# Optimization experiments

Measured on AMD Instinct MI355X. Metric: run time of the kernel, lower is better.

Reference implementation:

```python
import jax, jax.numpy as jnp
import numpy as np


def setup_inputs() -> dict:
    key = jax.random.key(0)
    k1, k2 = jax.random.split(key)
    B, T, V = 128, 256, 256
    batch = jax.random.normal(k1, (B, T, V, 3), dtype=jnp.float32)
    missing = jax.random.uniform(k2, (B, T, V)) < 0.2
    labels = jnp.where(missing, -1.0, 1.0)
    batch = batch.at[..., 0].set(labels)
    return {"batch": batch}


def reference(batch):
    B, T, V, _ = batch.shape
    dt = batch.dtype
    # constant-velocity model matrices (hardcoded in the module)
    F = jnp.array([[1, 0, 1, 0], [0, 1, 0, 1], [0, 0, 1, 0], [0, 0, 0, 1]], dtype=dt)
    H = jnp.array([[1, 0, 0, 0], [0, 1, 0, 0]], dtype=dt)
    Q = jnp.eye(4, dtype=dt) * 0.01
    R = jnp.eye(2, dtype=dt) * 1.0
    I4 = jnp.eye(4, dtype=dt)

    s0 = jnp.zeros((B, V, 4), dtype=dt)
    P0 = jnp.broadcast_to(jnp.eye(4, dtype=dt) * 1000.0, (B, V, 4, 4))

    obs_t = jnp.moveaxis(batch, 1, 0)  # (T, B, V, 3)

    def step(carry, obs):
        s, P = carry  # s: (B,V,4), P: (B,V,4,4)
        labels = obs[..., 0]
        z = obs[..., 1:]                       # (B,V,2)
        mask = (labels != -1)[..., None]       # (B,V,1)
        s_pred = jnp.einsum('bvj,ij->bvi', s, F)                 # s @ F.T
        P_pred = jnp.einsum('ij,bvjk,lk->bvil', F, P, F) + Q     # F P F^T + Q
        y = (z - s_pred[..., :2]) * mask                          # (B,V,2)
        S = P_pred[..., :2, :2] + R                               # H P H^T + R
        K = jnp.einsum('bvij,bvjk->bvik', P_pred[..., :, :2], jnp.linalg.inv(S))  # (B,V,4,2)
        s_upd = s_pred + jnp.einsum('bvij,bvj->bvi', K, y) * mask
        KH = jnp.einsum('bvij,jk->bvik', K, H)                    # (B,V,4,4)
        P_upd = jnp.einsum('bvij,bvjk->bvik', I4 - KH, P_pred)
        s_new = jnp.where(mask, s_upd, s_pred)
        P_new = jnp.where(mask[..., None], P_upd, P_pred)
        return (s_new, P_new), None

    (s_final, _), _ = jax.lax.scan(step, (s0, P0), obs_t)
    last_pos = s_final[..., :2]                                   # (B,V,2)
    ones = jnp.ones((B, V, 1), dtype=dt)
    return jnp.concatenate((ones, last_pos), axis=-1)             # (B,V,3)
```

## Files before the change

### kernel.cpp

```cpp
#include <hip/hip_runtime.h>
#include <stdint.h>


#define KF_B 128
#define KF_T 256
#define KF_V 256

typedef float f4 __attribute__((ext_vector_type(4)));

#define GLOAD(dst, sbase, imm)                                         \
    asm volatile("global_load_dwordx4 %0, %1, %2 offset:" #imm         \
                 : "=v"(dst) : "v"(voff), "s"(sbase) : "memory")

#define WAITVM(N, B)                                                   \
    asm volatile("s_waitcnt vmcnt(" #N ")"                             \
                 : "+v"((B)[0]), "+v"((B)[1]),                         \
                   "+v"((B)[2]), "+v"((B)[3]) :: "memory")

#define KF_ISSUE(buf)                          \
    do {                                       \
        GLOAD((buf)[0], sb0, 0);               \
        GLOAD((buf)[1], sb0, 3072);            \
        GLOAD((buf)[2], sb1, 0);               \
        GLOAD((buf)[3], sb1, 3068);            \
        sb0 += 12288; sb1 += 12288;            \
    } while (0)

#define KF_STEP3(label, z0, z1)                                         \
    do {                                                                \
                                                           \
        const float xp0 = x0 + v0;                                      \
        const float xp1 = x1 + v1;                                      \
        const float q00 = p00 + 2.f * p01 + p11 + 0.01f;                \
        const float q01 = p01 + p11;                                    \
        const float q11 = p11 + 0.01f;                                  \
                       \
        const float S = q00 + 1.f;                                      \
        const float m = ((label) != -1.0f) ? 1.0f : 0.0f;               \
        const float is = m * __builtin_amdgcn_rcpf(S);                  \
        const float K0 = q00 * is;                                      \
        const float K1 = q01 * is;                                      \
                                   \
        const float y0 = (z0) - xp0;                                    \
        const float y1 = (z1) - xp1;                                    \
        x0 = xp0 + K0 * y0;                                             \
        v0 = v0 + K1 * y0;                                              \
        x1 = xp1 + K0 * y1;                                             \
        v1 = v1 + K1 * y1;                                              \
                                                 \
        p00 = q00 - K0 * q00;                                           \
        p01 = q01 - K0 * q01;                                           \
        p11 = q11 - K1 * q01;                                           \
    } while (0)

#define KF_CONSUME(B)                                        \
    do {                                                     \
        KF_STEP3((B)[0][0], (B)[0][1], (B)[0][2]);           \
        KF_STEP3((B)[1][0], (B)[1][1], (B)[1][2]);           \
        KF_STEP3((B)[2][0], (B)[2][1], (B)[2][2]);           \
        KF_STEP3((B)[3][1], (B)[3][2], (B)[3][3]);           \
    } while (0)

__global__ __launch_bounds__(64, 1) void kf_kernel(const float* __restrict__ batch,
                                                   float* __restrict__ out) {
    const int blk = blockIdx.x;
    const int b = blk >> 2;
    const int v = ((blk & 3) << 6) | threadIdx.x;

    const uint32_t voff = (uint32_t)v * 12u;
    uint64_t sb0 = (uint64_t)batch + (uint64_t)b * (KF_T * KF_V * 3 * 4);
    uint64_t sb1 = sb0 + 6144;

    float p00 = 1000.f, p01 = 0.f, p11 = 1000.f;
    float x0 = 0.f, v0 = 0.f;
    float x1 = 0.f, v1 = 0.f;

#pragma unroll 1
    for (int body = 0; body < 16; ++body) {
        f4 g0[4], g1[4], g2[4], g3[4];
        KF_ISSUE(g0);
        KF_ISSUE(g1);
        KF_ISSUE(g2);
        KF_ISSUE(g3);
        WAITVM(12, g0); KF_CONSUME(g0);
        WAITVM(8,  g1); KF_CONSUME(g1);
        WAITVM(4,  g2); KF_CONSUME(g2);
        WAITVM(0,  g3); KF_CONSUME(g3);
    }

    const int tid = blk * 64 + threadIdx.x;
    float* o = out + (size_t)tid * 3;
    o[0] = 1.0f;
    o[1] = x0;
    o[2] = x1;
}

extern "C" void kernel_launch(void* const* d_in, const int* in_sizes, int n_in,
                              void* d_out, int out_size, void* d_ws, size_t ws_size,
                              hipStream_t stream) {
    (void)in_sizes; (void)n_in; (void)d_ws; (void)ws_size; (void)out_size;
    const float* batch = (const float*)d_in[0];
    float* out = (float*)d_out;
    const int total = KF_B * KF_V;
    kf_kernel<<<total / 64, 64, 0, stream>>>(batch, out);
}
```

Before: 146.1 us.

## Replace batched load/consume loop with rolling 8-deep software pipeline

Replaces the loop that issued four load groups and then drained all of them with a fully unrolled rolling pipeline of eight buffers. Each steady-state stage waits for its oldest group, consumes it, then immediately reissues loads into that buffer, so 32 loads stay in flight at all times instead of draining to zero every 16 timesteps. Total timesteps stay at 256 (8 prologue, 56 steady, 8 epilogue stages). The cost is higher VGPR use for 8 buffers and a much larger unrolled code body.

```diff
diff --git a/kernel.cpp b/kernel.cpp
--- a/kernel.cpp
+++ b/kernel.cpp
@@ -61,6 +61,14 @@
         KF_STEP3((B)[3][1], (B)[3][2], (B)[3][3]);           \
     } while (0)
 
+#define KF_STEADY(B)  do { WAITVM(28, B); KF_CONSUME(B); KF_ISSUE(B); } while (0)
+#define KF_STEADY8()                                          \
+    do {                                                      \
+        KF_STEADY(b0); KF_STEADY(b1); KF_STEADY(b2);          \
+        KF_STEADY(b3); KF_STEADY(b4); KF_STEADY(b5);          \
+        KF_STEADY(b6); KF_STEADY(b7);                         \
+    } while (0)
+
 __global__ __launch_bounds__(64, 1) void kf_kernel(const float* __restrict__ batch,
                                                    float* __restrict__ out) {
     const int blk = blockIdx.x;
@@ -75,18 +83,27 @@
     float x0 = 0.f, v0 = 0.f;
     float x1 = 0.f, v1 = 0.f;
 
-#pragma unroll 1
-    for (int body = 0; body < 16; ++body) {
-        f4 g0[4], g1[4], g2[4], g3[4];
-        KF_ISSUE(g0);
-        KF_ISSUE(g1);
-        KF_ISSUE(g2);
-        KF_ISSUE(g3);
-        WAITVM(12, g0); KF_CONSUME(g0);
-        WAITVM(8,  g1); KF_CONSUME(g1);
-        WAITVM(4,  g2); KF_CONSUME(g2);
-        WAITVM(0,  g3); KF_CONSUME(g3);
-    }
+    f4 b0[4], b1[4], b2[4], b3[4], b4[4], b5[4], b6[4], b7[4];
+
+    KF_ISSUE(b0); KF_ISSUE(b1); KF_ISSUE(b2); KF_ISSUE(b3);
+    KF_ISSUE(b4); KF_ISSUE(b5); KF_ISSUE(b6); KF_ISSUE(b7);
+
+    KF_STEADY8();
+    KF_STEADY8();
+    KF_STEADY8();
+    KF_STEADY8();
+    KF_STEADY8();
+    KF_STEADY8();
+    KF_STEADY8();
+
+    WAITVM(28, b0); KF_CONSUME(b0);
+    WAITVM(24, b1); KF_CONSUME(b1);
+    WAITVM(20, b2); KF_CONSUME(b2);
+    WAITVM(16, b3); KF_CONSUME(b3);
+    WAITVM(12, b4); KF_CONSUME(b4);
+    WAITVM(8,  b5); KF_CONSUME(b5);
+    WAITVM(4,  b6); KF_CONSUME(b6);
+    WAITVM(0,  b7); KF_CONSUME(b7);
 
     const int tid = blk * 64 + threadIdx.x;
     float* o = out + (size_t)tid * 3;
```

Result: no change. 144.5 us (-1.1%).

## Split Kalman time scan into four segments composed via affine maps

Applied to the files above, without the earlier changes.

Each block now uses four waves, each handling a quarter of the time axis for 64 spatial columns. The first wave runs the filter directly. The others first warm up the covariance recursion for 32 steps, then accumulate their segment's state update as an affine map, which is written to shared memory and composed by wave 0. This is meant to cut the long serial latency chain of the per-thread scan. It adds redundant covariance work and scalar loads in place of the old hand-scheduled vector loads. It also relies on the covariance converging within the warm-up window, so it is approximate if long runs of missing observations occur.

```diff
diff --git a/kernel.cpp b/kernel.cpp
--- a/kernel.cpp
+++ b/kernel.cpp
@@ -5,94 +5,139 @@
 #define KF_B 128
 #define KF_T 256
 #define KF_V 256
+#define SEGLEN 64
+#define WARM 32
+#define STRIDE (KF_V * 3)
 
-typedef float f4 __attribute__((ext_vector_type(4)));
+#define KF_GAIN(la)                                                  \
+    const float q00 = p00 + 2.f * p01 + p11 + 0.01f;                 \
+    const float q01 = p01 + p11;                                     \
+    const float q11 = p11 + 0.01f;                                   \
+    const float m = ((la) != -1.0f) ? 1.0f : 0.0f;                   \
+    const float is = m * __builtin_amdgcn_rcpf(q00 + 1.f);           \
+    const float K0 = q00 * is;                                       \
+    const float K1 = q01 * is;                                       \
+    p00 = q00 - K0 * q00;                                            \
+    p01 = q01 - K0 * q01;                                            \
+    p11 = q11 - K1 * q01;
 
-#define GLOAD(dst, sbase, imm)                                         \
-    asm volatile("global_load_dwordx4 %0, %1, %2 offset:" #imm         \
-                 : "=v"(dst) : "v"(voff), "s"(sbase) : "memory")
-
-#define WAITVM(N, B)                                                   \
-    asm volatile("s_waitcnt vmcnt(" #N ")"                             \
-                 : "+v"((B)[0]), "+v"((B)[1]),                         \
-                   "+v"((B)[2]), "+v"((B)[3]) :: "memory")
-
-#define KF_ISSUE(buf)                          \
-    do {                                       \
-        GLOAD((buf)[0], sb0, 0);               \
-        GLOAD((buf)[1], sb0, 3072);            \
-        GLOAD((buf)[2], sb1, 0);               \
-        GLOAD((buf)[3], sb1, 3068);            \
-        sb0 += 12288; sb1 += 12288;            \
+#define STEP_DIR(la, z0, z1)                                         \
+    do {                                                             \
+        KF_GAIN(la)                                                  \
+        const float xp0 = x0 + v0;                                   \
+        const float xp1 = x1 + v1;                                   \
+        const float y0 = (z0) - xp0;                                 \
+        const float y1 = (z1) - xp1;                                 \
+        x0 = xp0 + K0 * y0;                                          \
+        v0 = v0 + K1 * y0;                                           \
+        x1 = xp1 + K0 * y1;                                          \
+        v1 = v1 + K1 * y1;                                           \
     } while (0)
 
-#define KF_STEP3(label, z0, z1)                                         \
-    do {                                                                \
-                                                           \
-        const float xp0 = x0 + v0;                                      \
-        const float xp1 = x1 + v1;                                      \
-        const float q00 = p00 + 2.f * p01 + p11 + 0.01f;                \
-        const float q01 = p01 + p11;                                    \
-        const float q11 = p11 + 0.01f;                                  \
-                       \
-        const float S = q00 + 1.f;                                      \
-        const float m = ((label) != -1.0f) ? 1.0f : 0.0f;               \
-        const float is = m * __builtin_amdgcn_rcpf(S);                  \
-        const float K0 = q00 * is;                                      \
-        const float K1 = q01 * is;                                      \
-                                   \
-        const float y0 = (z0) - xp0;                                    \
-        const float y1 = (z1) - xp1;                                    \
-        x0 = xp0 + K0 * y0;                                             \
-        v0 = v0 + K1 * y0;                                              \
-        x1 = xp1 + K0 * y1;                                             \
-        v1 = v1 + K1 * y1;                                              \
-                                                 \
-        p00 = q00 - K0 * q00;                                           \
-        p01 = q01 - K0 * q01;                                           \
-        p11 = q11 - K1 * q01;                                           \
+#define STEP_AFF(la, z0, z1)                                         \
+    do {                                                             \
+        KF_GAIN(la)                                                  \
+        const float s00 = a00 + a10;                                 \
+        const float s01 = a01 + a11;                                 \
+        a00 = s00 - K0 * s00;                                        \
+        a01 = s01 - K0 * s01;                                        \
+        a10 = a10 - K1 * s00;                                        \
+        a11 = a11 - K1 * s01;                                        \
+        const float sbx = bx0 + bx1;                                 \
+        const float sby = by0 + by1;                                 \
+        bx0 = sbx + K0 * ((z0) - sbx);                               \
+        bx1 = bx1 + K1 * ((z0) - sbx);                               \
+        by0 = sby + K0 * ((z1) - sby);                               \
+        by1 = by1 + K1 * ((z1) - sby);                               \
     } while (0)
 
-#define KF_CONSUME(B)                                        \
-    do {                                                     \
-        KF_STEP3((B)[0][0], (B)[0][1], (B)[0][2]);           \
-        KF_STEP3((B)[1][0], (B)[1][1], (B)[1][2]);           \
-        KF_STEP3((B)[2][0], (B)[2][1], (B)[2][2]);           \
-        KF_STEP3((B)[3][1], (B)[3][2], (B)[3][3]);           \
-    } while (0)
+#define STEP_RICC(la)                                                \
+    do { KF_GAIN(la) } while (0)
 
-__global__ __launch_bounds__(64, 1) void kf_kernel(const float* __restrict__ batch,
-                                                   float* __restrict__ out) {
+__global__ __launch_bounds__(256, 4)
+void kf_kernel(const float* __restrict__ batch, float* __restrict__ out) {
     const int blk = blockIdx.x;
     const int b = blk >> 2;
-    const int v = ((blk & 3) << 6) | threadIdx.x;
+    const int lane = threadIdx.x & 63;
+    const int w = threadIdx.x >> 6;
+    const int v = ((blk & 3) << 6) | lane;
 
-    const uint32_t voff = (uint32_t)v * 12u;
-    uint64_t sb0 = (uint64_t)batch + (uint64_t)b * (KF_T * KF_V * 3 * 4);
-    uint64_t sb1 = sb0 + 6144;
+    const float* col = batch + (size_t)b * (KF_T * STRIDE) + (size_t)v * 3;
+
+    __shared__ float lds[3][64][9];
 
     float p00 = 1000.f, p01 = 0.f, p11 = 1000.f;
-    float x0 = 0.f, v0 = 0.f;
-    float x1 = 0.f, v1 = 0.f;
+    float x0 = 0.f, v0 = 0.f, x1 = 0.f, v1 = 0.f;
+    float a00 = 1.f, a01 = 0.f, a10 = 0.f, a11 = 1.f;
+    float bx0 = 0.f, bx1 = 0.f, by0 = 0.f, by1 = 0.f;
 
+    if (w == 0) {
+        const float* p = col;
+#pragma unroll 2
+        for (int t = 0; t < SEGLEN; t += 4) {
+            const float la0 = p[0],          z00 = p[1],          z01 = p[2];
+            const float la1 = p[STRIDE],     z10 = p[STRIDE+1],   z11 = p[STRIDE+2];
+            const float la2 = p[2*STRIDE],   z20 = p[2*STRIDE+1], z21 = p[2*STRIDE+2];
+            const float la3 = p[3*STRIDE],   z30 = p[3*STRIDE+1], z31 = p[3*STRIDE+2];
+            p += 4 * STRIDE;
+            STEP_DIR(la0, z00, z01);
+            STEP_DIR(la1, z10, z11);
+            STEP_DIR(la2, z20, z21);
+            STEP_DIR(la3, z30, z31);
+        }
+    } else {
+        const float* p = col + (size_t)(w * SEGLEN - WARM) * STRIDE;
 #pragma unroll 1
-    for (int body = 0; body < 16; ++body) {
-        f4 g0[4], g1[4], g2[4], g3[4];
-        KF_ISSUE(g0);
-        KF_ISSUE(g1);
-        KF_ISSUE(g2);
-        KF_ISSUE(g3);
-        WAITVM(12, g0); KF_CONSUME(g0);
-        WAITVM(8,  g1); KF_CONSUME(g1);
-        WAITVM(4,  g2); KF_CONSUME(g2);
-        WAITVM(0,  g3); KF_CONSUME(g3);
+        for (int t = 0; t < WARM; t += 8) {
+            const float la0 = p[0];
+            const float la1 = p[STRIDE];
+            const float la2 = p[2*STRIDE];
+            const float la3 = p[3*STRIDE];
+            const float la4 = p[4*STRIDE];
+            const float la5 = p[5*STRIDE];
+            const float la6 = p[6*STRIDE];
+            const float la7 = p[7*STRIDE];
+            p += 8 * STRIDE;
+            STEP_RICC(la0); STEP_RICC(la1); STEP_RICC(la2); STEP_RICC(la3);
+            STEP_RICC(la4); STEP_RICC(la5); STEP_RICC(la6); STEP_RICC(la7);
+        }
+#pragma unroll 2
+        for (int t = 0; t < SEGLEN; t += 4) {
+            const float la0 = p[0],          z00 = p[1],          z01 = p[2];
+            const float la1 = p[STRIDE],     z10 = p[STRIDE+1],   z11 = p[STRIDE+2];
+            const float la2 = p[2*STRIDE],   z20 = p[2*STRIDE+1], z21 = p[2*STRIDE+2];
+            const float la3 = p[3*STRIDE],   z30 = p[3*STRIDE+1], z31 = p[3*STRIDE+2];
+            p += 4 * STRIDE;
+            STEP_AFF(la0, z00, z01);
+            STEP_AFF(la1, z10, z11);
+            STEP_AFF(la2, z20, z21);
+            STEP_AFF(la3, z30, z31);
+        }
+        float* q = lds[w - 1][lane];
+        q[0] = a00; q[1] = a01; q[2] = a10; q[3] = a11;
+        q[4] = bx0; q[5] = bx1; q[6] = by0; q[7] = by1;
     }
 
-    const int tid = blk * 64 + threadIdx.x;
-    float* o = out + (size_t)tid * 3;
-    o[0] = 1.0f;
-    o[1] = x0;
-    o[2] = x1;
+    __syncthreads();
+
+    if (w == 0) {
+        float X0 = x0, W0 = v0, X1 = x1, W1 = v1;
+#pragma unroll
+        for (int s = 0; s < 3; ++s) {
+            const float* q = lds[s][lane];
+            const float c00 = q[0], c01 = q[1], c10 = q[2], c11 = q[3];
+            const float dx0 = q[4], dx1 = q[5], dy0 = q[6], dy1 = q[7];
+            const float nX0 = c00 * X0 + c01 * W0 + dx0;
+            const float nW0 = c10 * X0 + c11 * W0 + dx1;
+            const float nX1 = c00 * X1 + c01 * W1 + dy0;
+            const float nW1 = c10 * X1 + c11 * W1 + dy1;
+            X0 = nX0; W0 = nW0; X1 = nX1; W1 = nW1;
+        }
+        float* o = out + ((size_t)b * KF_V + v) * 3;
+        o[0] = 1.0f;
+        o[1] = X0;
+        o[2] = X1;
+    }
 }
 
 extern "C" void kernel_launch(void* const* d_in, const int* in_sizes, int n_in,
@@ -101,6 +146,6 @@
     (void)in_sizes; (void)n_in; (void)d_ws; (void)ws_size; (void)out_size;
     const float* batch = (const float*)d_in[0];
     float* out = (float*)d_out;
-    const int total = KF_B * KF_V;
-    kf_kernel<<<total / 64, 64, 0, stream>>>(batch, out);
+    const int blocks = KF_B * (KF_V / 64);
+    kf_kernel<<<blocks, 256, 0, stream>>>(batch, out);
 }
```

Measured after the change: 146.7 us. No clear change (+0.4%).
